# Optimization experiments

Hardware: AMD Instinct MI355X
Metric: run time of the kernel (lower is better)

Reference implementation:

```python
import jax, jax.numpy as jnp
import numpy as np

B, N, D, L, K, H = 64, 576, 768, 64, 5, 8  # batch, tokens, dim, out_token_len, knn k, heads
HD = D // H
SCALE = HD ** -0.5


def layer_norm(x, g, b, eps=1e-5):
    m = jnp.mean(x, axis=-1, keepdims=True)
    v = jnp.mean((x - m) ** 2, axis=-1, keepdims=True)
    return (x - m) * jax.lax.rsqrt(v + eps) * g + b


def cluster(feat, noise):
    # DPC-KNN: pairwise distances, k-NN density, parent distance, peak selection
    sq = jnp.sum(feat * feat, axis=-1)  # [B,N]
    dm = sq[:, :, None] + sq[:, None, :] - 2.0 * jnp.einsum('bnd,bmd->bnm', feat, feat)
    dm = jnp.sqrt(jnp.maximum(dm, 0.0)) / jnp.sqrt(jnp.asarray(D, feat.dtype))  # [B,N,N]
    neg_near, _ = jax.lax.top_k(-dm, K)                       # k smallest distances (negated)
    density = jnp.exp(-jnp.mean(neg_near ** 2, axis=-1))      # [B,N]
    density = density + noise * 1e-6                          # deterministic tie-break
    mask = (density[:, None, :] > density[:, :, None]).astype(feat.dtype)
    dist_max = jnp.max(dm.reshape(dm.shape[0], -1), axis=-1)[:, None, None]
    dist = jnp.min(dm * mask + dist_max * (1.0 - mask), axis=-1)  # [B,N]
    score = dist * density
    _, idx_down = jax.lax.top_k(score, L)                     # [B,L] cluster centers
    dm_down = jnp.take_along_axis(dm, idx_down[:, :, None], axis=1)  # [B,L,N]
    idx_cluster = jnp.argmin(dm_down, axis=1)                 # [B,N] assign to nearest center
    idx_cluster = idx_cluster.at[jnp.arange(dm.shape[0])[:, None], idx_down].set(
        jnp.arange(L)[None, :])
    return idx_cluster


def merger(feat, idx_cluster, token_score):
    b, n, d = feat.shape
    idx = (idx_cluster + jnp.arange(b)[:, None] * L).reshape(-1)       # [B*N]
    tw = jnp.exp(token_score)                                          # [B,N,1]
    all_w = jax.ops.segment_sum(tw.reshape(-1, 1), idx, num_segments=b * L) + 1e-6
    norm_w = tw / all_w[idx].reshape(b, n, 1)
    merged = jax.ops.segment_sum((feat * norm_w).reshape(-1, d), idx, num_segments=b * L)
    return merged.reshape(b, L, d)


def setup_inputs() -> dict:
    key = jax.random.key(0)
    ks = jax.random.split(key, 16)
    s = 0.02
    return {
        'x': jax.random.normal(ks[0], (B, N, D), jnp.float32),
        'density_noise': jax.random.uniform(ks[1], (B, N), jnp.float32),
        'norm1_g': jnp.ones((D,), jnp.float32),
        'norm1_b': jnp.zeros((D,), jnp.float32),
        'score_w': s * jax.random.normal(ks[2], (D, 1), jnp.float32),
        'score_b': jnp.zeros((1,), jnp.float32),
        'wq': s * jax.random.normal(ks[3], (D, D), jnp.float32),
        'wk': s * jax.random.normal(ks[4], (D, D), jnp.float32),
        'wv': s * jax.random.normal(ks[5], (D, D), jnp.float32),
        'proj_w': s * jax.random.normal(ks[6], (D, D), jnp.float32),
        'proj_b': jnp.zeros((D,), jnp.float32),
        'norm2_g': jnp.ones((D,), jnp.float32),
        'norm2_b': jnp.zeros((D,), jnp.float32),
        'fc1_w': s * jax.random.normal(ks[7], (D, 4 * D), jnp.float32),
        'fc1_b': jnp.zeros((4 * D,), jnp.float32),
        'fc2_w': s * jax.random.normal(ks[8], (4 * D, D), jnp.float32),
        'fc2_b': jnp.zeros((D,), jnp.float32),
    }


def reference(x, density_noise, norm1_g, norm1_b, score_w, score_b, wq, wk, wv,
              proj_w, proj_b, norm2_g, norm2_b, fc1_w, fc1_b, fc2_w, fc2_b):
    xn = layer_norm(x, norm1_g, norm1_b)                 # [B,N,D]
    token_score = xn @ score_w + score_b                 # [B,N,1]
    idx_cluster = cluster(jax.lax.stop_gradient(xn), density_noise)  # no-grad in torch
    q_input = merger(xn, idx_cluster, token_score)       # [B,L,D]
    kv = xn
    # STMAttention: cross-attn with token_score bias added to logits
    q = (q_input @ wq).reshape(B, L, H, HD).transpose(0, 2, 1, 3)
    k = (kv @ wk).reshape(B, N, H, HD).transpose(0, 2, 1, 3)
    v = (kv @ wv).reshape(B, N, H, HD).transpose(0, 2, 1, 3)
    dots = jnp.einsum('bhid,bhjd->bhij', q, k) * SCALE   # [B,H,L,N]
    bias = token_score[:, :, 0][:, None, None, :]        # [B,1,1,N]
    attn = jax.nn.softmax(dots + bias, axis=-1)
    out = jnp.einsum('bhij,bhjd->bhid', attn, v)
    out = out.transpose(0, 2, 1, 3).reshape(B, L, D)
    out = out @ proj_w + proj_b
    feature = q_input + out
    h = layer_norm(feature, norm2_g, norm2_b)
    h = jax.nn.gelu(h @ fc1_w + fc1_b, approximate=False) @ fc2_w + fc2_b
    return feature + h
```

## Files before the change

### kernel.cpp

```cpp
#include <hip/hip_runtime.h>
#include <math.h>

#define B_   64
#define N_   576
#define D_   768
#define L_   64
#define H_   8
#define HD_  96
#define NB_  (B_*N_)
#define ML_  (B_*L_)
#define KV_STRIDE_ 1536
#define SCALE_ 0.10206207f
#define INV_SQRT_D_ 0.03608439182f
#define LO_SCALE_ 4.8828125e-4f

typedef __attribute__((ext_vector_type(8))) _Float16 half8v;
typedef __attribute__((ext_vector_type(4))) float floatx4;

__device__ __forceinline__ unsigned short f2h(float f) {
  _Float16 h = (_Float16)f;
  unsigned short u; __builtin_memcpy(&u, &h, 2);
  return u;
}
__device__ __forceinline__ float h2f(unsigned short u) {
  _Float16 h; __builtin_memcpy(&h, &u, 2);
  return (float)h;
}
__device__ __forceinline__ void gload_lds16(const void* g, void* l) {
  __builtin_amdgcn_global_load_lds(
      (const __attribute__((address_space(1))) unsigned*)g,
      (__attribute__((address_space(3))) unsigned*)l, 16, 0, 0);
}

__global__ __launch_bounds__(256) void k_ln1(const float* __restrict__ x,
    const float* __restrict__ g, const float* __restrict__ bt,
    const float* __restrict__ sw, const float* __restrict__ sb,
    unsigned short* __restrict__ xh, unsigned short* __restrict__ xl,
    float* __restrict__ ts, float* __restrict__ sq)
{
  int row = blockIdx.x, tid = threadIdx.x;
  const float* xr = x + (size_t)row * D_;
  float v0 = xr[tid], v1 = xr[tid + 256], v2 = xr[tid + 512];
  __shared__ float r1[256], r2[256];
  r1[tid] = v0 + v1 + v2;
  r2[tid] = v0 * v0 + v1 * v1 + v2 * v2;
  __syncthreads();
  for (int o = 128; o > 0; o >>= 1) {
    if (tid < o) { r1[tid] += r1[tid + o]; r2[tid] += r2[tid + o]; }
    __syncthreads();
  }
  float mean = r1[0] * (1.0f / D_);
  float var  = r2[0] * (1.0f / D_) - mean * mean;
  float rstd = rsqrtf(var + 1e-5f);
  __syncthreads();
  float o0 = (v0 - mean) * rstd * g[tid      ] + bt[tid      ];
  float o1 = (v1 - mean) * rstd * g[tid + 256] + bt[tid + 256];
  float o2 = (v2 - mean) * rstd * g[tid + 512] + bt[tid + 512];
  auto split = [](float o, unsigned short& hu, unsigned short& lu) {
    _Float16 h = (_Float16)o;
    float hf = (float)h;
    _Float16 l = (_Float16)((o - hf) * 2048.0f);
    __builtin_memcpy(&hu, &h, 2);
    __builtin_memcpy(&lu, &l, 2);
  };
  unsigned short h0, l0, h1, l1, h2, l2;
  split(o0, h0, l0); split(o1, h1, l1); split(o2, h2, l2);
  unsigned short* xho = xh + (size_t)row * D_;
  unsigned short* xlo = xl + (size_t)row * D_;
  xho[tid] = h0; xho[tid + 256] = h1; xho[tid + 512] = h2;
  xlo[tid] = l0; xlo[tid + 256] = l1; xlo[tid + 512] = l2;
  r1[tid] = o0 * sw[tid] + o1 * sw[tid + 256] + o2 * sw[tid + 512];
  r2[tid] = o0 * o0 + o1 * o1 + o2 * o2;
  __syncthreads();
  for (int o = 128; o > 0; o >>= 1) {
    if (tid < o) { r1[tid] += r1[tid + o]; r2[tid] += r2[tid + o]; }
    __syncthreads();
  }
  if (tid == 0) { ts[row] = r1[0] + sb[0]; sq[row] = r2[0]; }
}

__global__ __launch_bounds__(256) void k_dmg(const unsigned short* __restrict__ xh,
    const unsigned short* __restrict__ xl, const float* __restrict__ sq,
    float* __restrict__ dm, float* __restrict__ dmax)
{
  __shared__ __align__(16) unsigned short S[4][96 * 64];
  int b = blockIdx.y;
  int t = blockIdx.x, ti = 0, rl = 6;
  while (t >= rl) { t -= rl; ++ti; --rl; }
  int tj = ti + t;
  int tid = threadIdx.x;
  int wave = tid >> 6, lane = tid & 63;
  int wr = (wave >> 1) * 48, wc = (wave & 1) * 48;
  int mloc = lane & 15, quad = lane >> 4;
  size_t rowA = (size_t)b * N_ + ti * 96;
  size_t rowB = (size_t)b * N_ + tj * 96;

  const unsigned short* srcbase =
      (wave == 0) ? xh + rowA * D_ :
      (wave == 1) ? xl + rowA * D_ :
      (wave == 2) ? xh + rowB * D_ : xl + rowB * D_;
  int lrow = lane >> 3, lchunk = lane & 7;
  const unsigned short* gsrc0 = srcbase + (size_t)lrow * D_ + ((lchunk ^ lrow) * 8);
  unsigned short* lbase = &S[wave][0];

  floatx4 a1[3][3], a2[3][3];
#pragma unroll
  for (int i = 0; i < 3; ++i)
#pragma unroll
    for (int j = 0; j < 3; ++j) {
      a1[i][j] = (floatx4){0.f, 0.f, 0.f, 0.f};
      a2[i][j] = (floatx4){0.f, 0.f, 0.f, 0.f};
    }

  for (int kt = 0; kt < D_; kt += 64) {
    __syncthreads();
#pragma unroll
    for (int rb = 0; rb < 12; ++rb)
      gload_lds16(gsrc0 + (size_t)rb * 8 * D_ + kt, lbase + rb * 8 * 64);
    __syncthreads();
#pragma unroll
    for (int ks = 0; ks < 2; ++ks) {
      half8v ah[3], al[3], bh[3], bl[3];
      int cperm = (((ks << 2) | quad) ^ (mloc & 7)) * 8;
#pragma unroll
      for (int i = 0; i < 3; ++i) {
        int ro = (wr + i * 16 + mloc) * 64 + cperm;
        ah[i] = *(const half8v*)&S[0][ro];
        al[i] = *(const half8v*)&S[1][ro];
      }
#pragma unroll
      for (int j = 0; j < 3; ++j) {
        int ro = (wc + j * 16 + mloc) * 64 + cperm;
        bh[j] = *(const half8v*)&S[2][ro];
        bl[j] = *(const half8v*)&S[3][ro];
      }
#pragma unroll
      for (int i = 0; i < 3; ++i)
#pragma unroll
        for (int j = 0; j < 3; ++j) {
          a1[i][j] = __builtin_amdgcn_mfma_f32_16x16x32_f16(ah[i], bh[j], a1[i][j], 0, 0, 0);
          a2[i][j] = __builtin_amdgcn_mfma_f32_16x16x32_f16(ah[i], bl[j], a2[i][j], 0, 0, 0);
          a2[i][j] = __builtin_amdgcn_mfma_f32_16x16x32_f16(al[i], bh[j], a2[i][j], 0, 0, 0);
        }
    }
  }

  const float* sqb = sq + b * N_;
  float* dmb = dm + (size_t)b * N_ * N_;
  bool diag = (ti == tj);
  float vmax = 0.f;
#pragma unroll
  for (int j = 0; j < 3; ++j) {
    int gj = tj * 96 + wc + j * 16 + mloc;
    float sj = sqb[gj];
#pragma unroll
    for (int i = 0; i < 3; ++i) {
      int gi0 = ti * 96 + wr + i * 16 + quad * 4;
#pragma unroll
      for (int reg = 0; reg < 4; ++reg) {
        int gi = gi0 + reg;
        float g = a1[i][j][reg] + a2[i][j][reg] * LO_SCALE_;
        float d = sqb[gi] + sj - 2.0f * g;
        float v = sqrtf(fmaxf(d, 0.0f)) * INV_SQRT_D_;
        vmax = fmaxf(vmax, v);
        if (!diag || gj >= gi) {
          dmb[(size_t)gi * N_ + gj] = v;
          dmb[(size_t)gj * N_ + gi] = v;
        }
      }
    }
  }
#pragma unroll
  for (int msk = 32; msk >= 1; msk >>= 1) vmax = fmaxf(vmax, __shfl_xor(vmax, msk));
  if (lane == 0) atomicMax((unsigned int*)(dmax + b), __float_as_uint(vmax));
}

__global__ __launch_bounds__(64) void k_density(const float* __restrict__ dm,
    const float* __restrict__ noise, float* __restrict__ den)
{
  int row = blockIdx.x, lane = threadIdx.x;
  const float* r = dm + (size_t)row * N_;
  float a0 = 1e30f, a1 = 1e30f, a2 = 1e30f, a3 = 1e30f, a4 = 1e30f;
  auto ins5 = [&](float xv) {
    a4 = fminf(a4, xv);
    float t;
    t = fminf(a3, a4); a4 = fmaxf(a3, a4); a3 = t;
    t = fminf(a2, a3); a3 = fmaxf(a2, a3); a2 = t;
    t = fminf(a1, a2); a2 = fmaxf(a1, a2); a1 = t;
    t = fminf(a0, a1); a1 = fmaxf(a0, a1); a0 = t;
  };
#pragma unroll
  for (int t = 0; t < 9; ++t) ins5(r[lane + 64 * t]);
  for (int m = 1; m < 64; m <<= 1) {
    float b0 = __shfl_xor(a0, m), b1 = __shfl_xor(a1, m), b2 = __shfl_xor(a2, m);
    float b3 = __shfl_xor(a3, m), b4 = __shfl_xor(a4, m);
    ins5(b0); ins5(b1); ins5(b2); ins5(b3); ins5(b4);
  }
  if (lane == 0) {
    float ms = (a0 * a0 + a1 * a1 + a2 * a2 + a3 * a3 + a4 * a4) * 0.2f;
    den[row] = expf(-ms) + noise[row] * 1e-6f;
  }
}

__global__ __launch_bounds__(64) void k_dist(const float* __restrict__ dm,
    const float* __restrict__ den, const float* __restrict__ dmax,
    float* __restrict__ score)
{
  int row = blockIdx.x, lane = threadIdx.x;
  int b = row / N_;
  float di = den[row], dx = dmax[b];
  const float* r = dm + (size_t)row * N_;
  const float* db = den + b * N_;
  float m = dx;
#pragma unroll
  for (int t = 0; t < 9; ++t) {
    int j = lane + 64 * t;
    float v = (db[j] > di) ? r[j] : dx;
    m = fminf(m, v);
  }
  for (int msk = 1; msk < 64; msk <<= 1) m = fminf(m, __shfl_xor(m, msk));
  if (lane == 0) score[row] = m * di;
}

__global__ __launch_bounds__(256) void k_topL(const float* __restrict__ score,
    int* __restrict__ idxd)
{
  int b = blockIdx.x, tid = threadIdx.x;
  __shared__ float s[N_];
  __shared__ float rv[256];
  __shared__ int   ri[256];
  for (int j = tid; j < N_; j += 256) s[j] = score[b * N_ + j];
  __syncthreads();
  for (int it = 0; it < L_; ++it) {
    float bv = -1e30f; int bi = 1 << 30;
    for (int j = tid; j < N_; j += 256) {
      float v = s[j];
      if (v > bv || (v == bv && j < bi)) { bv = v; bi = j; }
    }
    rv[tid] = bv; ri[tid] = bi; __syncthreads();
    for (int o = 128; o > 0; o >>= 1) {
      if (tid < o) {
        float v2 = rv[tid + o]; int i2 = ri[tid + o];
        if (v2 > rv[tid] || (v2 == rv[tid] && i2 < ri[tid])) { rv[tid] = v2; ri[tid] = i2; }
      }
      __syncthreads();
    }
    if (tid == 0) { idxd[b * L_ + it] = ri[0]; s[ri[0]] = -1e30f; }
    __syncthreads();
  }
}

__global__ __launch_bounds__(576) void k_assign(const float* __restrict__ dm,
    const int* __restrict__ idxd, int* __restrict__ idxc)
{
  int b = blockIdx.x, n = threadIdx.x;
  __shared__ int ctr[L_];
  if (n < L_) ctr[n] = idxd[b * L_ + n];
  __syncthreads();
  const float* dmb = dm + (size_t)b * N_ * N_;
  float best = 1e30f; int bl = 0;
  for (int l = 0; l < L_; ++l) {
    float v = dmb[(size_t)ctr[l] * N_ + n];
    if (v < best) { best = v; bl = l; }
  }
  for (int l = 0; l < L_; ++l)
    if (ctr[l] == n) bl = l;
  idxc[b * N_ + n] = bl;
}

__global__ __launch_bounds__(256) void k_merge(const unsigned short* __restrict__ xh,
    const unsigned short* __restrict__ xl,
    const float* __restrict__ ts, const int* __restrict__ idxc,
    float* __restrict__ qin)
{
  int blk = blockIdx.x;
  int b = blk >> 6, l = blk & 63;
  int tid = threadIdx.x;
  const int* ic = idxc + b * N_;
  const float* tsb = ts + b * N_;
  const unsigned short* xhb = xh + (size_t)b * N_ * D_;
  const unsigned short* xlb = xl + (size_t)b * N_ * D_;
  float a0 = 0.f, a1 = 0.f, a2 = 0.f, wsum = 0.f;
  for (int n = 0; n < N_; ++n) {
    if (ic[n] == l) {
      float w = expf(tsb[n]);
      wsum += w;
      const unsigned short* hr = xhb + (size_t)n * D_;
      const unsigned short* lr = xlb + (size_t)n * D_;
      float x0 = h2f(hr[tid      ]) + h2f(lr[tid      ]) * LO_SCALE_;
      float x1 = h2f(hr[tid + 256]) + h2f(lr[tid + 256]) * LO_SCALE_;
      float x2 = h2f(hr[tid + 512]) + h2f(lr[tid + 512]) * LO_SCALE_;
      a0 += w * x0; a1 += w * x1; a2 += w * x2;
    }
  }
  float inv = 1.0f / (wsum + 1e-6f);
  float* q = qin + (size_t)blk * D_;
  q[tid] = a0 * inv; q[tid + 256] = a1 * inv; q[tid + 512] = a2 * inv;
}

__global__ __launch_bounds__(256) void k_wt(const float* __restrict__ W,
    unsigned short* __restrict__ WT, int K, int N)
{
  __shared__ float t[32][33];
  int k0 = blockIdx.x * 32, n0 = blockIdx.y * 32;
  int tid = threadIdx.x;
  int r = tid >> 3, c4 = (tid & 7) * 4;
  float4 v = *(const float4*)(W + (size_t)(k0 + r) * N + n0 + c4);
  t[r][c4] = v.x; t[r][c4 + 1] = v.y; t[r][c4 + 2] = v.z; t[r][c4 + 3] = v.w;
  __syncthreads();
  ushort4 s4;
  s4.x = f2h(t[c4 + 0][r]); s4.y = f2h(t[c4 + 1][r]);
  s4.z = f2h(t[c4 + 2][r]); s4.w = f2h(t[c4 + 3][r]);
  *(ushort4*)(WT + (size_t)(n0 + r) * K + k0 + c4) = s4;
}

template<int EPI, int ASRC>
__global__ __launch_bounds__(256) void k_mgemm(const void* __restrict__ Ap_,
    const unsigned short* __restrict__ Wt, const float* __restrict__ bias,
    const float* __restrict__ res, void* __restrict__ outp,
    int M, int Nd, int Kd)
{
  constexpr int APITCH = (ASRC == 1) ? 32 : 40;
  __shared__ __align__(16) unsigned short As[128 * APITCH];
  __shared__ __align__(16) unsigned short Bs[128 * 32];
  int tid = threadIdx.x;
  int bm = blockIdx.x * 128, bn = blockIdx.y * 128;
  int wave = tid >> 6, lane = tid & 63;
  int wr = (wave >> 1) * 64, wc = (wave & 1) * 64;
  int mloc = lane & 15, quad = lane >> 4;

  floatx4 acc[4][4];
#pragma unroll
  for (int i = 0; i < 4; ++i)
#pragma unroll
    for (int j = 0; j < 4; ++j)
      acc[i][j] = (floatx4){0.f, 0.f, 0.f, 0.f};

  int gr = wave * 32 + (lane >> 2);
  int gc = (lane & 3) * 8;

  for (int kt = 0; kt < Kd; kt += 32) {
    __syncthreads();
#pragma unroll
    for (int rb = 0; rb < 2; ++rb)
      gload_lds16(Wt + (size_t)(bn + gr + rb * 16) * Kd + kt + gc,
                  &Bs[(wave * 32 + rb * 16) * 32]);
    if (ASRC == 1) {
      const unsigned short* A = (const unsigned short*)Ap_;
#pragma unroll
      for (int rb = 0; rb < 2; ++rb)
        gload_lds16(A + (size_t)(bm + gr + rb * 16) * Kd + kt + gc,
                    &As[(wave * 32 + rb * 16) * 32]);
    } else {
      const float* A = (const float*)Ap_;
#pragma unroll
      for (int it = 0; it < 2; ++it) {
        int idx = tid + it * 256;
        int r = idx >> 2, c = idx & 3;
        const float* ap = A + (size_t)(bm + r) * Kd + kt + c * 8;
        float4 f0 = *(const float4*)ap;
        float4 f1 = *(const float4*)(ap + 4);
        uint4 pk;
        pk.x = (unsigned)f2h(f0.x) | ((unsigned)f2h(f0.y) << 16);
        pk.y = (unsigned)f2h(f0.z) | ((unsigned)f2h(f0.w) << 16);
        pk.z = (unsigned)f2h(f1.x) | ((unsigned)f2h(f1.y) << 16);
        pk.w = (unsigned)f2h(f1.z) | ((unsigned)f2h(f1.w) << 16);
        *(uint4*)&As[r * 40 + c * 8] = pk;
      }
    }
    __syncthreads();
    half8v af[4], bf[4];
#pragma unroll
    for (int i = 0; i < 4; ++i)
      af[i] = *(const half8v*)&As[(wr + i * 16 + mloc) * APITCH + quad * 8];
#pragma unroll
    for (int j = 0; j < 4; ++j)
      bf[j] = *(const half8v*)&Bs[(wc + j * 16 + mloc) * 32 + quad * 8];
#pragma unroll
    for (int i = 0; i < 4; ++i)
#pragma unroll
      for (int j = 0; j < 4; ++j)
        acc[i][j] = __builtin_amdgcn_mfma_f32_16x16x32_f16(af[i], bf[j], acc[i][j], 0, 0, 0);
  }

  float bv[4] = {0.f, 0.f, 0.f, 0.f};
  if (EPI >= 1) {
#pragma unroll
    for (int j = 0; j < 4; ++j) bv[j] = bias[bn + wc + j * 16 + mloc];
  }
#pragma unroll
  for (int i = 0; i < 4; ++i) {
    int gr0 = bm + wr + i * 16 + quad * 4;
#pragma unroll
    for (int j = 0; j < 4; ++j) {
      int gcn = bn + wc + j * 16 + mloc;
#pragma unroll
      for (int reg = 0; reg < 4; ++reg) {
        float v = acc[i][j][reg];
        size_t off = (size_t)(gr0 + reg) * Nd + gcn;
        if (EPI == 0) {
          ((unsigned short*)outp)[off] = f2h(v);
        } else if (EPI == 1) {
          ((float*)outp)[off] = v + bv[j] + res[off];
        } else {
          v += bv[j];
          v = 0.5f * v * (1.0f + erff(v * 0.70710678f));
          ((unsigned short*)outp)[off] = f2h(v);
        }
      }
    }
  }
}

__global__ __launch_bounds__(256) void k_attn(const unsigned short* __restrict__ Qu,
    const unsigned short* __restrict__ KVu, const float* __restrict__ ts,
    float* __restrict__ aout)
{
  __shared__ __align__(16) unsigned short Ks[64 * 104];
  __shared__ __align__(16) unsigned short VsT[96 * 64];
  __shared__ __align__(16) unsigned short sPa[64 * 64];
  __shared__ float tsb[64];
  int h = blockIdx.x, b = blockIdx.y;
  int tid = threadIdx.x;
  int wave = tid >> 6, lane = tid & 63;
  int mloc = lane & 15, quad = lane >> 4;

  half8v qf[3];
  {
    const unsigned short* qrow = Qu + (size_t)(b * 64 + wave * 16 + mloc) * D_ + h * 96 + quad * 8;
#pragma unroll
    for (int k = 0; k < 3; ++k) qf[k] = *(const half8v*)(qrow + k * 32);
  }

  floatx4 of[6];
#pragma unroll
  for (int dt = 0; dt < 6; ++dt) of[dt] = (floatx4){0.f, 0.f, 0.f, 0.f};
  float m[4], l[4];
#pragma unroll
  for (int r = 0; r < 4; ++r) { m[r] = -1e30f; l[r] = 0.f; }

  for (int jt = 0; jt < 9; ++jt) {
    int j0 = jt * 64;
    __syncthreads();
#pragma unroll
    for (int t = 0; t < 3; ++t) {
      int id = tid + t * 256;
      int row = id / 12, c = id % 12;
      *(uint4*)&Ks[row * 104 + c * 8] =
          *(const uint4*)(KVu + (size_t)(b * N_ + j0 + row) * KV_STRIDE_ + h * 96 + c * 8);
    }
#pragma unroll
    for (int t = 0; t < 3; ++t) {
      int id = tid + t * 256;
      int keyp = id & 31, dq = (id >> 5) * 4;
      int key = keyp * 2;
      const unsigned short* vp =
          KVu + (size_t)(b * N_ + j0 + key) * KV_STRIDE_ + 768 + h * 96 + dq;
      ushort4 v0 = *(const ushort4*)vp;
      ushort4 v1 = *(const ushort4*)(vp + KV_STRIDE_);
      unsigned pk0 = (unsigned)v0.x | ((unsigned)v1.x << 16);
      unsigned pk1 = (unsigned)v0.y | ((unsigned)v1.y << 16);
      unsigned pk2 = (unsigned)v0.z | ((unsigned)v1.z << 16);
      unsigned pk3 = (unsigned)v0.w | ((unsigned)v1.w << 16);
      int cbase = key >> 3, off = key & 7;
#pragma unroll
      for (int i = 0; i < 4; ++i) {
        int d = dq + i;
        unsigned pv = (i == 0) ? pk0 : (i == 1) ? pk1 : (i == 2) ? pk2 : pk3;
        *(unsigned*)&VsT[d * 64 + ((cbase ^ (d & 7)) << 3) + off] = pv;
      }
    }
    if (tid < 64) tsb[tid] = ts[b * N_ + j0 + tid];
    __syncthreads();

    floatx4 acc[4];
#pragma unroll
    for (int j = 0; j < 4; ++j) acc[j] = (floatx4){0.f, 0.f, 0.f, 0.f};
#pragma unroll
    for (int j = 0; j < 4; ++j)
#pragma unroll
      for (int k = 0; k < 3; ++k) {
        half8v kf = *(const half8v*)&Ks[(j * 16 + mloc) * 104 + k * 32 + quad * 8];
        acc[j] = __builtin_amdgcn_mfma_f32_16x16x32_f16(qf[k], kf, acc[j], 0, 0, 0);
      }

    float ts4[4];
#pragma unroll
    for (int j = 0; j < 4; ++j) ts4[j] = tsb[j * 16 + mloc];
    float rm[4] = {-1e30f, -1e30f, -1e30f, -1e30f};
#pragma unroll
    for (int j = 0; j < 4; ++j)
#pragma unroll
      for (int r = 0; r < 4; ++r) {
        acc[j][r] = acc[j][r] * SCALE_ + ts4[j];
        rm[r] = fmaxf(rm[r], acc[j][r]);
      }
#pragma unroll
    for (int r = 0; r < 4; ++r) {
      rm[r] = fmaxf(rm[r], __shfl_xor(rm[r], 1));
      rm[r] = fmaxf(rm[r], __shfl_xor(rm[r], 2));
      rm[r] = fmaxf(rm[r], __shfl_xor(rm[r], 4));
      rm[r] = fmaxf(rm[r], __shfl_xor(rm[r], 8));
    }
    float alpha[4], rs[4];
#pragma unroll
    for (int r = 0; r < 4; ++r) {
      float mn = fmaxf(m[r], rm[r]);
      alpha[r] = __expf(m[r] - mn);
      m[r] = mn;
      rs[r] = 0.f;
    }
#pragma unroll
    for (int j = 0; j < 4; ++j)
#pragma unroll
      for (int r = 0; r < 4; ++r) {
        float p = __expf(acc[j][r] - m[r]);
        acc[j][r] = p; rs[r] += p;
      }
#pragma unroll
    for (int r = 0; r < 4; ++r) {
      rs[r] += __shfl_xor(rs[r], 1); rs[r] += __shfl_xor(rs[r], 2);
      rs[r] += __shfl_xor(rs[r], 4); rs[r] += __shfl_xor(rs[r], 8);
      l[r] = l[r] * alpha[r] + rs[r];
    }
#pragma unroll
    for (int dt = 0; dt < 6; ++dt)
#pragma unroll
      for (int r = 0; r < 4; ++r) of[dt][r] *= alpha[r];

#pragma unroll
    for (int j = 0; j < 4; ++j)
#pragma unroll
      for (int r = 0; r < 4; ++r) {
        int row = wave * 16 + quad * 4 + r;
        int key = j * 16 + mloc;
        sPa[row * 64 + (((key >> 3) ^ (row & 7)) << 3) + (key & 7)] = f2h(acc[j][r]);
      }
    half8v pa[2];
    int prow = wave * 16 + mloc;
#pragma unroll
    for (int f2 = 0; f2 < 2; ++f2)
      pa[f2] = *(const half8v*)&sPa[prow * 64 + (((f2 * 4 + quad) ^ (prow & 7)) << 3)];
#pragma unroll
    for (int dt = 0; dt < 6; ++dt)
#pragma unroll
      for (int f2 = 0; f2 < 2; ++f2) {
        int vrow = dt * 16 + mloc;
        half8v vf = *(const half8v*)&VsT[vrow * 64 + (((f2 * 4 + quad) ^ (vrow & 7)) << 3)];
        of[dt] = __builtin_amdgcn_mfma_f32_16x16x32_f16(pa[f2], vf, of[dt], 0, 0, 0);
      }
  }

  float linv[4];
#pragma unroll
  for (int r = 0; r < 4; ++r) linv[r] = 1.0f / l[r];
#pragma unroll
  for (int dt = 0; dt < 6; ++dt)
#pragma unroll
    for (int r = 0; r < 4; ++r) {
      int row = b * 64 + wave * 16 + quad * 4 + r;
      int col = h * 96 + dt * 16 + mloc;
      aout[(size_t)row * D_ + col] = of[dt][r] * linv[r];
    }
}

__global__ __launch_bounds__(256) void k_ln2(const float* __restrict__ f,
    const float* __restrict__ g, const float* __restrict__ bt, float* __restrict__ out)
{
  int row = blockIdx.x, tid = threadIdx.x;
  const float* fr = f + (size_t)row * D_;
  float v0 = fr[tid], v1 = fr[tid + 256], v2 = fr[tid + 512];
  __shared__ float r1[256], r2[256];
  r1[tid] = v0 + v1 + v2;
  r2[tid] = v0 * v0 + v1 * v1 + v2 * v2;
  __syncthreads();
  for (int o = 128; o > 0; o >>= 1) {
    if (tid < o) { r1[tid] += r1[tid + o]; r2[tid] += r2[tid + o]; }
    __syncthreads();
  }
  float mean = r1[0] * (1.0f / D_);
  float var  = r2[0] * (1.0f / D_) - mean * mean;
  float rstd = rsqrtf(var + 1e-5f);
  float* oo = out + (size_t)row * D_;
  oo[tid      ] = (v0 - mean) * rstd * g[tid      ] + bt[tid      ];
  oo[tid + 256] = (v1 - mean) * rstd * g[tid + 256] + bt[tid + 256];
  oo[tid + 512] = (v2 - mean) * rstd * g[tid + 512] + bt[tid + 512];
}

extern "C" void kernel_launch(void* const* d_in, const int* in_sizes, int n_in,
                              void* d_out, int out_size, void* d_ws, size_t ws_size,
                              hipStream_t stream)
{
  (void)in_sizes; (void)n_in; (void)out_size; (void)ws_size;
  const float* x    = (const float*)d_in[0];
  const float* nois = (const float*)d_in[1];
  const float* n1g  = (const float*)d_in[2];
  const float* n1b  = (const float*)d_in[3];
  const float* sw   = (const float*)d_in[4];
  const float* sb   = (const float*)d_in[5];
  const float* wq   = (const float*)d_in[6];
  const float* wk   = (const float*)d_in[7];
  const float* wv   = (const float*)d_in[8];
  const float* pw   = (const float*)d_in[9];
  const float* pb   = (const float*)d_in[10];
  const float* n2g  = (const float*)d_in[11];
  const float* n2b  = (const float*)d_in[12];
  const float* f1w  = (const float*)d_in[13];
  const float* f1b  = (const float*)d_in[14];
  const float* f2w  = (const float*)d_in[15];
  const float* f2b  = (const float*)d_in[16];

  float* ws    = (float*)d_ws;
  unsigned short* XH = (unsigned short*)ws;
  unsigned short* XL = XH + (size_t)NB_ * D_;
  float* RG    = ws + (size_t)NB_ * D_;
  float* QIN   = RG + (size_t)NB_ * D_;
  float* FEAT  = QIN + (size_t)ML_ * D_;
  float* AOUT  = FEAT + (size_t)ML_ * D_;
  float* QBUF  = AOUT + (size_t)ML_ * D_;
  float* P     = QBUF + (size_t)ML_ * D_;
  unsigned short* QH16 = (unsigned short*)P;  P += (size_t)ML_ * D_ / 2;
  unsigned short* WTQ  = (unsigned short*)P;  P += (size_t)D_ * D_ / 2;
  unsigned short* WTKV = (unsigned short*)P;  P += (size_t)D_ * D_;
  unsigned short* WTP  = (unsigned short*)P;  P += (size_t)D_ * D_ / 2;
  unsigned short* WT1  = (unsigned short*)P;  P += (size_t)D_ * 4 * D_ / 2;
  unsigned short* WT2  = (unsigned short*)P;  P += (size_t)D_ * 4 * D_ / 2;
  float* TS    = P;
  float* SQ    = TS + NB_;
  float* DEN   = SQ + NB_;
  float* SCORE = DEN + NB_;
  float* DMAX  = SCORE + NB_;
  int*   IDXD  = (int*)(DMAX + 64);
  int*   IDXC  = IDXD + ML_;
  float* DM    = RG;
  unsigned short* KVB = (unsigned short*)RG;
  unsigned short* HID = (unsigned short*)RG;

  hipMemsetAsync(DMAX, 0, 64 * sizeof(float), stream);
  k_wt<<<dim3(24, 24), 256, 0, stream>>>(wq, WTQ, D_, D_);
  k_wt<<<dim3(24, 24), 256, 0, stream>>>(wk, WTKV, D_, D_);
  k_wt<<<dim3(24, 24), 256, 0, stream>>>(wv, WTKV + (size_t)D_ * D_, D_, D_);
  k_wt<<<dim3(24, 24), 256, 0, stream>>>(pw, WTP, D_, D_);
  k_wt<<<dim3(24, 96), 256, 0, stream>>>(f1w, WT1, D_, 4 * D_);
  k_wt<<<dim3(96, 24), 256, 0, stream>>>(f2w, WT2, 4 * D_, D_);

  k_ln1<<<NB_, 256, 0, stream>>>(x, n1g, n1b, sw, sb, XH, XL, TS, SQ);
  k_dmg<<<dim3(21, B_), 256, 0, stream>>>(XH, XL, SQ, DM, DMAX);
  k_density<<<NB_, 64, 0, stream>>>(DM, nois, DEN);
  k_dist<<<NB_, 64, 0, stream>>>(DM, DEN, DMAX, SCORE);
  k_topL<<<B_, 256, 0, stream>>>(SCORE, IDXD);
  k_assign<<<B_, 576, 0, stream>>>(DM, IDXD, IDXC);
  k_merge<<<ML_, 256, 0, stream>>>(XH, XL, TS, IDXC, QIN);

  k_mgemm<0, 0><<<dim3(ML_ / 128, D_ / 128), 256, 0, stream>>>(
      QIN, WTQ, nullptr, nullptr, QH16, ML_, D_, D_);
  k_mgemm<0, 1><<<dim3(NB_ / 128, KV_STRIDE_ / 128), 256, 0, stream>>>(
      XH, WTKV, nullptr, nullptr, KVB, NB_, KV_STRIDE_, D_);
  k_attn<<<dim3(H_, B_), 256, 0, stream>>>(QH16, KVB, TS, AOUT);
  k_mgemm<1, 0><<<dim3(ML_ / 128, D_ / 128), 256, 0, stream>>>(
      AOUT, WTP, pb, QIN, FEAT, ML_, D_, D_);
  k_ln2<<<ML_, 256, 0, stream>>>(FEAT, n2g, n2b, QBUF);
  k_mgemm<2, 0><<<dim3(ML_ / 128, (4 * D_) / 128), 256, 0, stream>>>(
      QBUF, WT1, f1b, nullptr, HID, ML_, 4 * D_, D_);
  k_mgemm<1, 1><<<dim3(ML_ / 128, D_ / 128), 256, 0, stream>>>(
      HID, WT2, f2b, FEAT, d_out, ML_, D_, 4 * D_);
}
```

Baseline: 992.5 us.

## Deepen GEMM K-tile to 64 with XOR-swizzled LDS layout

The fp16 MFMA GEMM now stages 64-wide K slices of A and W into LDS per iteration instead of 32, which halves the number of barrier-separated load phases. Shared-memory rows use an XOR swizzle on the 16-byte chunk index, replacing the previous padding, to avoid bank conflicts on the fragment reads. LDS use per block grows and the swizzled addressing adds some index arithmetic. Kd is assumed to be a multiple of 64.

After: 946.6 us. 1.05x faster.

```diff
diff --git a/kernel.cpp b/kernel.cpp
--- a/kernel.cpp
+++ b/kernel.cpp
@@ -320,9 +320,8 @@
     const float* __restrict__ res, void* __restrict__ outp,
     int M, int Nd, int Kd)
 {
-  constexpr int APITCH = (ASRC == 1) ? 32 : 40;
-  __shared__ __align__(16) unsigned short As[128 * APITCH];
-  __shared__ __align__(16) unsigned short Bs[128 * 32];
+  __shared__ __align__(16) unsigned short As[128 * 64];
+  __shared__ __align__(16) unsigned short Bs[128 * 64];
   int tid = threadIdx.x;
   int bm = blockIdx.x * 128, bn = blockIdx.y * 128;
   int wave = tid >> 6, lane = tid & 63;
@@ -336,27 +335,30 @@
     for (int j = 0; j < 4; ++j)
       acc[i][j] = (floatx4){0.f, 0.f, 0.f, 0.f};
 
-  int gr = wave * 32 + (lane >> 2);
-  int gc = (lane & 3) * 8;
-
-  for (int kt = 0; kt < Kd; kt += 32) {
-    __syncthreads();
-#pragma unroll
-    for (int rb = 0; rb < 2; ++rb)
-      gload_lds16(Wt + (size_t)(bn + gr + rb * 16) * Kd + kt + gc,
-                  &Bs[(wave * 32 + rb * 16) * 32]);
+  int lrow = lane >> 3, lchunk = lane & 7;
+  const unsigned short* bsrc0 =
+      Wt + (size_t)(bn + wave * 32 + lrow) * Kd + ((lchunk ^ lrow) * 8);
+  unsigned short* bdst0 = &Bs[(wave * 32) * 64];
+  const unsigned short* asrc0 = (ASRC == 1)
+      ? (const unsigned short*)Ap_ + (size_t)(bm + wave * 32 + lrow) * Kd + ((lchunk ^ lrow) * 8)
+      : nullptr;
+  unsigned short* adst0 = &As[(wave * 32) * 64];
+
+  for (int kt = 0; kt < Kd; kt += 64) {
+    __syncthreads();
+#pragma unroll
+    for (int rb = 0; rb < 4; ++rb)
+      gload_lds16(bsrc0 + (size_t)rb * 8 * Kd + kt, bdst0 + rb * 8 * 64);
     if (ASRC == 1) {
-      const unsigned short* A = (const unsigned short*)Ap_;
-#pragma unroll
-      for (int rb = 0; rb < 2; ++rb)
-        gload_lds16(A + (size_t)(bm + gr + rb * 16) * Kd + kt + gc,
-                    &As[(wave * 32 + rb * 16) * 32]);
+#pragma unroll
+      for (int rb = 0; rb < 4; ++rb)
+        gload_lds16(asrc0 + (size_t)rb * 8 * Kd + kt, adst0 + rb * 8 * 64);
     } else {
       const float* A = (const float*)Ap_;
 #pragma unroll
-      for (int it = 0; it < 2; ++it) {
+      for (int it = 0; it < 4; ++it) {
         int idx = tid + it * 256;
-        int r = idx >> 2, c = idx & 3;
+        int r = idx >> 3, c = idx & 7;
         const float* ap = A + (size_t)(bm + r) * Kd + kt + c * 8;
         float4 f0 = *(const float4*)ap;
         float4 f1 = *(const float4*)(ap + 4);
@@ -365,22 +367,26 @@
         pk.y = (unsigned)f2h(f0.z) | ((unsigned)f2h(f0.w) << 16);
         pk.z = (unsigned)f2h(f1.x) | ((unsigned)f2h(f1.y) << 16);
         pk.w = (unsigned)f2h(f1.z) | ((unsigned)f2h(f1.w) << 16);
-        *(uint4*)&As[r * 40 + c * 8] = pk;
-      }
-    }
-    __syncthreads();
-    half8v af[4], bf[4];
-#pragma unroll
-    for (int i = 0; i < 4; ++i)
-      af[i] = *(const half8v*)&As[(wr + i * 16 + mloc) * APITCH + quad * 8];
-#pragma unroll
-    for (int j = 0; j < 4; ++j)
-      bf[j] = *(const half8v*)&Bs[(wc + j * 16 + mloc) * 32 + quad * 8];
-#pragma unroll
-    for (int i = 0; i < 4; ++i)
+        *(uint4*)&As[r * 64 + ((c ^ (r & 7)) * 8)] = pk;
+      }
+    }
+    __syncthreads();
+#pragma unroll
+    for (int ks = 0; ks < 2; ++ks) {
+      half8v af[4], bf[4];
+      int cperm = (((ks << 2) | quad) ^ (mloc & 7)) * 8;
+#pragma unroll
+      for (int i = 0; i < 4; ++i)
+        af[i] = *(const half8v*)&As[(wr + i * 16 + mloc) * 64 + cperm];
 #pragma unroll
       for (int j = 0; j < 4; ++j)
-        acc[i][j] = __builtin_amdgcn_mfma_f32_16x16x32_f16(af[i], bf[j], acc[i][j], 0, 0, 0);
+        bf[j] = *(const half8v*)&Bs[(wc + j * 16 + mloc) * 64 + cperm];
+#pragma unroll
+      for (int i = 0; i < 4; ++i)
+#pragma unroll
+        for (int j = 0; j < 4; ++j)
+          acc[i][j] = __builtin_amdgcn_mfma_f32_16x16x32_f16(af[i], bf[j], acc[i][j], 0, 0, 0);
+    }
   }
 
   float bv[4] = {0.f, 0.f, 0.f, 0.f};
```
